# Optimization experiments

Measured on AMD Instinct MI355X. Metric: run time of the kernel, lower is better.

## Reference

```python
import jax, jax.numpy as jnp
import numpy as np

B, S, H = 4, 2048, 512
E, K = 8, 2
DFF = 4 * H


def setup_inputs() -> dict:
    key = jax.random.key(0)
    ks = jax.random.split(key, 6)
    x = jax.random.normal(ks[0], (B, S, H), dtype=jnp.float32)
    gate_W = jax.random.normal(ks[1], (H, E), dtype=jnp.float32) * 0.02
    gate_b = jnp.zeros((E,), dtype=jnp.float32)
    # Stacked expert params; Linear stored as [in, out] so y = x @ W + b
    W1 = jax.random.normal(ks[2], (E, H, DFF), dtype=jnp.float32) * 0.02
    b1 = jnp.zeros((E, DFF), dtype=jnp.float32)
    W2 = jax.random.normal(ks[3], (E, DFF, H), dtype=jnp.float32) * 0.02
    b2 = jnp.zeros((E, H), dtype=jnp.float32)
    return {"x": x, "gate_W": gate_W, "gate_b": gate_b,
            "W1": W1, "b1": b1, "W2": W2, "b2": b2}


def reference(x, gate_W, gate_b, W1, b1, W2, b2):
    bsz, seq, hid = x.shape
    flat = x.reshape(-1, hid)                       # [T, H]
    T = flat.shape[0]
    gate_logits = flat @ gate_W + gate_b            # [T, E]
    topk_vals, topk_idx = jax.lax.top_k(gate_logits, K)   # [T, K]
    topk_w = jax.nn.softmax(topk_vals, axis=-1)      # softmax over selected logits only

    # Scatter top-k weights into a dense per-token combine matrix [T, E];
    # zero weight where a token is not routed -> identical math to masked dispatch.
    combine = jnp.zeros((T, E), dtype=flat.dtype).at[
        jnp.arange(T)[:, None], topk_idx].add(topk_w)

    out_flat = jnp.zeros_like(flat)
    for e in range(E):  # fixed small loop over structurally distinct experts
        h = jax.nn.gelu(flat @ W1[e] + b1[e], approximate=False) @ W2[e] + b2[e]
        out_flat = out_flat + h * combine[:, e:e + 1]
    out = out_flat.reshape(bsz, seq, hid)

    probs = jax.nn.softmax(gate_logits, axis=-1).mean(axis=0)   # [E]
    l_aux = jnp.sum(probs * probs) * E
    expert_counts = jnp.zeros((E,), dtype=jnp.float32).at[
        topk_idx.reshape(-1)].add(1.0)
    return out, l_aux, expert_counts
```

## Files before the change

### kernel.cpp

```cpp
#include <hip/hip_runtime.h>
#include <math.h>

#define TOK 8192
#define HD  512
#define NE  8
#define DFF 2048

typedef __attribute__((ext_vector_type(8))) short bf16x8;
typedef __attribute__((ext_vector_type(4))) float floatx4;

__device__ inline unsigned short f2bf(float f) {
    union { float f; unsigned u; } v; v.f = f;
    unsigned r = v.u + 0x7FFFu + ((v.u >> 16) & 1u);
    return (unsigned short)(r >> 16);
}

__device__ inline float gelu_exact(float v) {
    return 0.5f * v * (1.f + erff(v * 0.70710678118654752f));
}

typedef __attribute__((address_space(1))) const unsigned int glb_u32;
typedef __attribute__((address_space(3))) unsigned int lds_u32;
__device__ __forceinline__ void gload16(const unsigned short* g, unsigned short* l) {
    __builtin_amdgcn_global_load_lds((glb_u32*)g, (lds_u32*)l, 16, 0, 0);
}

__global__ __launch_bounds__(256) void prep_kernel(
    const float* __restrict__ x, const float* __restrict__ gW, const float* __restrict__ gb,
    const float* __restrict__ W1, const float* __restrict__ W2,
    int* __restrict__ seg_count, float* __restrict__ probs_sum,
    int* __restrict__ seg_token, float* __restrict__ seg_w,
    unsigned short* __restrict__ xb,
    unsigned short* __restrict__ W1t, unsigned short* __restrict__ W2t)
{
    __shared__ __align__(16) char shraw[16896];
    int bid = blockIdx.x;
    int tid = threadIdx.x;

    if (bid >= 32) {
        int b = bid - 32;
        float (*tile)[65] = (float(*)[65])shraw;
        int z = b >> 8, rem = b & 255;
        int xq = rem & 31, yq = rem >> 5;
        const float* src; unsigned short* dst; int C, R, cb, rb;
        if (z < NE) {
            src = W1 + (size_t)z * HD * DFF; dst = W1t + (size_t)z * HD * DFF;
            R = HD; C = DFF; cb = xq; rb = yq;
        } else {
            int e = z - NE;
            src = W2 + (size_t)e * DFF * HD; dst = W2t + (size_t)e * DFF * HD;
            R = DFF; C = HD; cb = yq; rb = xq;
        }
        int c0 = cb * 64, r0 = rb * 64;
        int tq = (tid & 15) * 4, tr4 = tid >> 4;
        #pragma unroll
        for (int p = 0; p < 4; p++) {
            int rr = tr4 + 16 * p;
            float4 v = *(const float4*)&src[(size_t)(r0 + rr) * C + c0 + tq];
            tile[rr][tq + 0] = v.x; tile[rr][tq + 1] = v.y;
            tile[rr][tq + 2] = v.z; tile[rr][tq + 3] = v.w;
        }
        __syncthreads();
        int cc = tid >> 3, cq = (tid & 7) * 8;
        #pragma unroll
        for (int p = 0; p < 2; p++) {
            int c = cc + 32 * p;
            union { unsigned short s[8]; uint4 v; } u8;
            #pragma unroll
            for (int u = 0; u < 8; u++) u8.s[u] = f2bf(tile[cq + u][c]);
            *(uint4*)&dst[(size_t)(c0 + c) * R + r0 + cq] = u8.v;
        }
        return;
    }

    float* sW    = (float*)shraw;
    float* psum  = (float*)(shraw + 16384);
    int*   lcount = (int*)(shraw + 16448);
    int*   lbase  = (int*)(shraw + 16512);

    for (int i = tid; i < HD * NE; i += 256) sW[i] = gW[i];
    if (tid < NE) { psum[tid] = 0.f; lcount[tid] = 0; }
    __syncthreads();

    int t = bid * 256 + tid;
    float logit[NE];
    #pragma unroll
    for (int e = 0; e < NE; e++) logit[e] = gb[e];

    const float4* xr4 = reinterpret_cast<const float4*>(x + (size_t)t * HD);
    ushort4* xbw = reinterpret_cast<ushort4*>(xb + (size_t)t * HD);
    for (int j4 = 0; j4 < HD / 4; j4++) {
        float4 xv = xr4[j4];
        int j = j4 * 4;
        ushort4 o; o.x = f2bf(xv.x); o.y = f2bf(xv.y); o.z = f2bf(xv.z); o.w = f2bf(xv.w);
        xbw[j4] = o;
        #pragma unroll
        for (int e = 0; e < NE; e++) {
            logit[e] += xv.x * sW[(j + 0) * NE + e] + xv.y * sW[(j + 1) * NE + e]
                      + xv.z * sW[(j + 2) * NE + e] + xv.w * sW[(j + 3) * NE + e];
        }
    }

    float mx = logit[0];
    #pragma unroll
    for (int e = 1; e < NE; e++) mx = fmaxf(mx, logit[e]);
    float pe[NE]; float s = 0.f;
    #pragma unroll
    for (int e = 0; e < NE; e++) { pe[e] = expf(logit[e] - mx); s += pe[e]; }
    float inv = 1.f / s;
    int l = tid & 63;
    #pragma unroll
    for (int e = 0; e < NE; e++) {
        float v = pe[e] * inv;
        for (int off = 32; off; off >>= 1) v += __shfl_down(v, off);
        if (l == 0) atomicAdd(&psum[e], v);
    }

    int i0 = 0; float v0 = logit[0];
    #pragma unroll
    for (int e = 1; e < NE; e++) if (logit[e] > v0) { v0 = logit[e]; i0 = e; }
    int i1 = -1; float v1 = -3.4e38f;
    #pragma unroll
    for (int e = 0; e < NE; e++) if (e != i0 && logit[e] > v1) { v1 = logit[e]; i1 = e; }
    float e1 = expf(v1 - v0);
    float w0 = 1.f / (1.f + e1);
    float w1 = e1 / (1.f + e1);

    int r0 = atomicAdd(&lcount[i0], 1);
    int r1 = atomicAdd(&lcount[i1], 1);
    __syncthreads();
    if (tid < NE) lbase[tid] = atomicAdd(&seg_count[tid], lcount[tid]);
    __syncthreads();
    int p0 = lbase[i0] + r0;
    seg_token[i0 * TOK + p0] = t;
    seg_w[i0 * TOK + p0] = w0;
    int p1 = lbase[i1] + r1;
    seg_token[i1 * TOK + p1] = t | (1 << 16);
    seg_w[i1 * TOK + p1] = w1;

    __syncthreads();
    if (tid < NE) atomicAdd(&probs_sum[tid], psum[tid]);
}

#define TM  128
#define TN  128
#define BK  32

#define GEMM_BODY(NITV, SRC_A, SRC_B) \
    const int NIT = (NITV); \
    int rbuf = 0; \
    for (int k = 0; k < NIT; ++k) { \
        if (k + 1 < NIT) asm volatile("s_waitcnt vmcnt(8)" ::: "memory"); \
        else             asm volatile("s_waitcnt vmcnt(0)" ::: "memory"); \
        const unsigned short* A = &smem[w * 8192 + rbuf * 4096]; \
        const unsigned short* B = A + 2048; \
        bf16x8 a[4], b[4]; \
        _Pragma("unroll") \
        for (int i = 0; i < 4; i++) a[i] = *(const bf16x8*)&A[(16 * i + lr) * BK + rsw]; \
        _Pragma("unroll") \
        for (int j = 0; j < 4; j++) b[j] = *(const bf16x8*)&B[(16 * j + lr) * BK + rsw]; \
        asm volatile("s_waitcnt lgkmcnt(0)" ::: "memory"); \
        if (k + 2 < NIT) { \
            int ko = (k + 2) * BK; \
            unsigned short* da = &smem[w * 8192 + rbuf * 4096]; \
            _Pragma("unroll") \
            for (int s = 0; s < 4; s++) { \
                gload16(SRC_A + aofs[s] + ko, da + s * 512); \
                gload16(SRC_B + bofs[s] + ko, da + 2048 + s * 512); \
            } \
        } \
        __builtin_amdgcn_s_setprio(1); \
        _Pragma("unroll") \
        for (int i = 0; i < 4; i++) \
            _Pragma("unroll") \
            for (int j = 0; j < 4; j++) \
                acc[i][j] = __builtin_amdgcn_mfma_f32_16x16x32_bf16(a[i], b[j], acc[i][j], 0, 0, 0); \
        __builtin_amdgcn_s_setprio(0); \
        rbuf ^= 1; \
    }

__global__ __launch_bounds__(256) void gemm1_kernel(
    const unsigned short* __restrict__ xb,
    const unsigned short* __restrict__ W1t,
    const float* __restrict__ bias1,
    const int* __restrict__ seg_count, const float* __restrict__ probs_sum,
    const int* __restrict__ seg_token,
    unsigned short* __restrict__ hbuf,
    float* __restrict__ out_tail)
{
    int bid = blockIdx.x;
    int tid = threadIdx.x;

    if (bid == 0) {
        if (tid < NE) out_tail[1 + tid] = (float)seg_count[tid];
        else if (tid == 64) {
            float s = 0.f;
            #pragma unroll
            for (int e2 = 0; e2 < NE; e2++) {
                float p = probs_sum[e2] * (1.f / (float)TOK);
                s += p * p;
            }
            out_tail[0] = s * (float)NE;
        }
    }

    int e  = bid & 7;
    int r2 = bid >> 3;
    int nb = r2 & 15;
    int mb = r2 >> 4;
    int cnt = seg_count[e];
    if (mb * TM >= cnt) return;

    int off_e = 0;
    #pragma unroll
    for (int ee = 0; ee < NE; ee++) if (ee < e) off_e += (seg_count[ee] + 127) & ~127;
    int hb = off_e + mb * TM;

    __shared__ __align__(16) unsigned short smem[32768];

    int w = tid >> 6, l = tid & 63;
    int lr = l & 15, crow = (l >> 4) * 4;
    int wm = (w & 1) * 64, wn = (w >> 1) * 64;
    int rsw = ((l >> 4) ^ ((lr >> 1) & 3)) * 8;
    const unsigned short* w1e = W1t + (size_t)e * DFF * HD + (size_t)(nb * TN) * HD;

    unsigned csrc = (unsigned)(((l & 3) ^ ((l >> 3) & 3)) * 8);
    unsigned aofs[4], bofs[4];
    #pragma unroll
    for (int s = 0; s < 4; s++) {
        int rloc = s * 16 + (l >> 2);
        int gi = mb * TM + wm + rloc;
        int tok = seg_token[e * TOK + ((gi < cnt) ? gi : 0)] & 0xFFFF;
        aofs[s] = (unsigned)tok * HD + csrc;
        bofs[s] = (unsigned)((wn + rloc) * HD) + csrc;
    }

    floatx4 acc[4][4];
    #pragma unroll
    for (int i = 0; i < 4; i++)
        #pragma unroll
        for (int j = 0; j < 4; j++) acc[i][j] = (floatx4){0.f, 0.f, 0.f, 0.f};

    #pragma unroll
    for (int p = 0; p < 2; p++) {
        unsigned short* da = &smem[w * 8192 + p * 4096];
        #pragma unroll
        for (int s = 0; s < 4; s++) {
            gload16(xb  + aofs[s] + p * BK, da + s * 512);
            gload16(w1e + bofs[s] + p * BK, da + 2048 + s * 512);
        }
    }

    GEMM_BODY(HD / BK, xb, w1e)

    unsigned short* scr = &smem[w * 8192];
    #pragma unroll
    for (int j = 0; j < 4; j++) {
        float b1v = bias1[e * DFF + nb * TN + wn + 16 * j + lr];
        #pragma unroll
        for (int i = 0; i < 4; i++)
            #pragma unroll
            for (int rr = 0; rr < 4; rr++)
                scr[(16 * i + crow + rr) * 72 + 16 * j + lr] = f2bf(gelu_exact(acc[i][j][rr] + b1v));
    }
    int lh = l >> 3, ll = l & 7;
    #pragma unroll
    for (int k = 0; k < 8; k++) {
        uint4 v = *(const uint4*)&scr[(8 * k + lh) * 72 + ll * 8];
        int grow = hb + wm + 8 * k + lh;
        *(uint4*)&hbuf[(size_t)grow * DFF + nb * TN + wn + ll * 8] = v;
    }
}

__global__ __launch_bounds__(256) void gemm2_kernel(
    const unsigned short* __restrict__ hbuf,
    const unsigned short* __restrict__ W2t,
    const float* __restrict__ b2,
    const int* __restrict__ seg_count, const int* __restrict__ seg_token,
    const float* __restrict__ seg_w,
    float* __restrict__ pout,
    float* __restrict__ out,
    int use_pout)
{
    int bid = blockIdx.x;
    int tid = threadIdx.x;
    int e  = bid & 7;
    int r2 = bid >> 3;
    int nb = r2 & 3;
    int mb = r2 >> 2;
    int cnt = seg_count[e];
    if (mb * TM >= cnt) return;
    int off_e = 0;
    #pragma unroll
    for (int ee = 0; ee < NE; ee++) if (ee < e) off_e += (seg_count[ee] + 127) & ~127;
    int hb = off_e + mb * TM;

    __shared__ __align__(16) unsigned short smem[32768];

    int w = tid >> 6, l = tid & 63;
    int lr = l & 15, crow = (l >> 4) * 4;
    int wm = (w & 1) * 64, wn = (w >> 1) * 64;
    int rsw = ((l >> 4) ^ ((lr >> 1) & 3)) * 8;
    const unsigned short* w2e = W2t + (size_t)e * HD * DFF + (size_t)(nb * TN) * DFF;

    unsigned csrc = (unsigned)(((l & 3) ^ ((l >> 3) & 3)) * 8);
    unsigned aofs[4], bofs[4];
    #pragma unroll
    for (int s = 0; s < 4; s++) {
        int rloc = s * 16 + (l >> 2);
        aofs[s] = (unsigned)((hb + wm + rloc) * DFF) + csrc;
        bofs[s] = (unsigned)((wn + rloc) * DFF) + csrc;
    }

    floatx4 acc[4][4];
    #pragma unroll
    for (int i = 0; i < 4; i++)
        #pragma unroll
        for (int j = 0; j < 4; j++) acc[i][j] = (floatx4){0.f, 0.f, 0.f, 0.f};

    #pragma unroll
    for (int p = 0; p < 2; p++) {
        unsigned short* da = &smem[w * 8192 + p * 4096];
        #pragma unroll
        for (int s = 0; s < 4; s++) {
            gload16(hbuf + aofs[s] + p * BK, da + s * 512);
            gload16(w2e  + bofs[s] + p * BK, da + 2048 + s * 512);
        }
    }

    GEMM_BODY(DFF / BK, hbuf, w2e)

    int   raws[4][4];
    float wgts[4][4];
    #pragma unroll
    for (int i = 0; i < 4; i++)
        #pragma unroll
        for (int rr = 0; rr < 4; rr++) {
            int gi = mb * TM + wm + 16 * i + crow + rr;
            int idx = e * TOK + ((gi < cnt) ? gi : 0);
            raws[i][rr] = seg_token[idx];
            wgts[i][rr] = (gi < cnt) ? seg_w[idx] : 0.f;
        }

    if (use_pout) {
        #pragma unroll
        for (int j = 0; j < 4; j++) {
            int n = nb * TN + wn + 16 * j + lr;
            float b2v = b2[e * HD + n];
            #pragma unroll
            for (int i = 0; i < 4; i++)
                #pragma unroll
                for (int rr = 0; rr < 4; rr++) {
                    int gi = mb * TM + wm + 16 * i + crow + rr;
                    if (gi < cnt)
                        pout[((size_t)(raws[i][rr] & 0xFFFF) * 2 + (raws[i][rr] >> 16)) * HD + n] =
                            (acc[i][j][rr] + b2v) * wgts[i][rr];
                }
        }
    } else {
        #pragma unroll
        for (int j = 0; j < 4; j++) {
            int n = nb * TN + wn + 16 * j + lr;
            float b2v = b2[e * HD + n];
            #pragma unroll
            for (int i = 0; i < 4; i++)
                #pragma unroll
                for (int rr = 0; rr < 4; rr++)
                    atomicAdd(&out[(size_t)(raws[i][rr] & 0xFFFF) * HD + n],
                              (acc[i][j][rr] + b2v) * wgts[i][rr]);
        }
    }
}

__global__ __launch_bounds__(256) void combine_kernel(
    const float* __restrict__ pout, float* __restrict__ out)
{
    int idx = blockIdx.x * 256 + threadIdx.x;
    int t = idx >> 7;
    int c4 = idx & 127;
    const float4* p = (const float4*)pout;
    float4 a = p[((size_t)t * 2 + 0) * 128 + c4];
    float4 b = p[((size_t)t * 2 + 1) * 128 + c4];
    float4 r; r.x = a.x + b.x; r.y = a.y + b.y; r.z = a.z + b.z; r.w = a.w + b.w;
    ((float4*)out)[idx] = r;
}

#define BMT 64
#define FK  64
#define XS_LD 520
#define HS_LD 72

__global__ __launch_bounds__(256, 2) void ffn_fused_fallback(
    const unsigned short* __restrict__ xb,
    const unsigned short* __restrict__ W1t, const float* __restrict__ b1,
    const unsigned short* __restrict__ W2t, const float* __restrict__ b2,
    const int* __restrict__ seg_count, const int* __restrict__ seg_token,
    const float* __restrict__ seg_w, float* __restrict__ out)
{
    int bid = blockIdx.x;
    int e = bid & 7;
    int g = bid >> 3;
    int cnt = seg_count[e];
    int n0 = g * BMT;
    if (n0 >= cnt) return;
    int rows = min(BMT, cnt - n0);

    __shared__ unsigned short xs[BMT * XS_LD];
    __shared__ unsigned short hs[BMT * HS_LD];
    __shared__ int   tok_s[BMT];
    __shared__ float wgt_s[BMT];

    int tid = threadIdx.x;
    if (tid < BMT) {
        int idx = (tid < rows) ? (n0 + tid) : n0;
        tok_s[tid] = seg_token[e * TOK + idx] & 0xFFFF;
        wgt_s[tid] = (tid < rows) ? seg_w[e * TOK + idx] : 0.f;
    }
    __syncthreads();
    {
        int r = tid >> 2, q = tid & 3;
        const uint4* src = (const uint4*)(xb + (size_t)tok_s[r] * HD) + q * 16;
        uint4* dst = (uint4*)&xs[(size_t)r * XS_LD + q * 128];
        #pragma unroll
        for (int i = 0; i < 16; i++) dst[i] = src[i];
    }
    __syncthreads();

    int w = tid >> 6, l = tid & 63;
    int lr = l & 15, lk = (l >> 4) * 8, crow = (l >> 4) * 4;

    const unsigned short* w1e = W1t + (size_t)e * DFF * HD;
    const unsigned short* w2e = W2t + (size_t)e * HD * DFF;

    floatx4 acc2[4][8];
    #pragma unroll
    for (int i = 0; i < 4; i++)
        #pragma unroll
        for (int j = 0; j < 8; j++) acc2[i][j] = (floatx4){0.f, 0.f, 0.f, 0.f};

    for (int fc = 0; fc < DFF; fc += FK) {
        floatx4 acc1[4];
        #pragma unroll
        for (int t = 0; t < 4; t++) acc1[t] = (floatx4){0.f, 0.f, 0.f, 0.f};
        const unsigned short* w1c = w1e + (size_t)fc * HD;
        for (int ks = 0; ks < HD; ks += 32) {
            bf16x8 a = *(const bf16x8*)&xs[(16 * w + lr) * XS_LD + ks + lk];
            #pragma unroll
            for (int t = 0; t < 4; t++) {
                bf16x8 b = *(const bf16x8*)(w1c + (size_t)(16 * t + lr) * HD + ks + lk);
                acc1[t] = __builtin_amdgcn_mfma_f32_16x16x32_bf16(a, b, acc1[t], 0, 0, 0);
            }
        }
        __syncthreads();
        #pragma unroll
        for (int t = 0; t < 4; t++) {
            float b1v = b1[e * DFF + fc + 16 * t + lr];
            #pragma unroll
            for (int r = 0; r < 4; r++)
                hs[(16 * w + crow + r) * HS_LD + 16 * t + lr] = f2bf(gelu_exact(acc1[t][r] + b1v));
        }
        __syncthreads();
        #pragma unroll
        for (int ks = 0; ks < FK; ks += 32) {
            bf16x8 af[4];
            #pragma unroll
            for (int i = 0; i < 4; i++) af[i] = *(const bf16x8*)&hs[(16 * i + lr) * HS_LD + ks + lk];
            #pragma unroll
            for (int j = 0; j < 8; j++) {
                bf16x8 b = *(const bf16x8*)(w2e + (size_t)(128 * w + 16 * j + lr) * DFF + fc + ks + lk);
                #pragma unroll
                for (int i = 0; i < 4; i++)
                    acc2[i][j] = __builtin_amdgcn_mfma_f32_16x16x32_bf16(af[i], b, acc2[i][j], 0, 0, 0);
            }
        }
    }
    #pragma unroll
    for (int j = 0; j < 8; j++) {
        int n = 128 * w + 16 * j + lr;
        float b2v = b2[e * HD + n];
        #pragma unroll
        for (int i = 0; i < 4; i++)
            #pragma unroll
            for (int r = 0; r < 4; r++) {
                int m = 16 * i + crow + r;
                atomicAdd(&out[(size_t)tok_s[m] * HD + n], (acc2[i][j][r] + b2v) * wgt_s[m]);
            }
    }
}

__global__ void finalize_kernel(const int* __restrict__ seg_count,
                                const float* __restrict__ probs_sum,
                                float* __restrict__ out_tail)
{
    int tid = threadIdx.x;
    if (tid < NE) out_tail[1 + tid] = (float)seg_count[tid];
    if (tid == 0) {
        float s = 0.f;
        #pragma unroll
        for (int e = 0; e < NE; e++) {
            float p = probs_sum[e] * (1.f / (float)TOK);
            s += p * p;
        }
        out_tail[0] = s * (float)NE;
    }
}

extern "C" void kernel_launch(void* const* d_in, const int* in_sizes, int n_in,
                              void* d_out, int out_size, void* d_ws, size_t ws_size,
                              hipStream_t stream)
{
    const float* x  = (const float*)d_in[0];
    const float* gW = (const float*)d_in[1];
    const float* gb = (const float*)d_in[2];
    const float* W1 = (const float*)d_in[3];
    const float* b1 = (const float*)d_in[4];
    const float* W2 = (const float*)d_in[5];
    const float* b2 = (const float*)d_in[6];
    float* out = (float*)d_out;

    char* ws = (char*)d_ws;
    int*   seg_count = (int*)ws;
    float* probs_sum = (float*)(ws + 32);
    int*   seg_token = (int*)(ws + 4096);
    float* seg_w     = (float*)(ws + 4096 + (size_t)NE * TOK * 4);

    const size_t HBUF_BYTES = (size_t)17408 * DFF * 2;

    const size_t F_POUT = 0xA0000;
    const size_t F_XB   = (1u  << 20);
    const size_t F_W1T  = (9u  << 20);
    const size_t F_W2T  = F_POUT + (size_t)TOK * 2 * HD * 4;
    const size_t F_HBUF = F_W2T + ((size_t)NE * DFF * HD * 2);
    const size_t WS_FAST = F_HBUF + HBUF_BYTES;

    const size_t M_XB   = (1u  << 20);
    const size_t M_W1T  = (16u << 20);
    const size_t M_W2T  = (32u << 20);
    const size_t M_HBUF = (48u << 20);
    const size_t WS_MID = M_HBUF + HBUF_BYTES;

    hipMemsetAsync(d_ws, 0, 64, stream);

    if (ws_size >= WS_FAST) {
        unsigned short* xb   = (unsigned short*)(ws + F_XB);
        unsigned short* W1t  = (unsigned short*)(ws + F_W1T);
        unsigned short* W2t  = (unsigned short*)(ws + F_W2T);
        unsigned short* hbuf = (unsigned short*)(ws + F_HBUF);
        float*          pout = (float*)(ws + F_POUT);

        prep_kernel<<<4128, 256, 0, stream>>>(x, gW, gb, W1, W2,
                                              seg_count, probs_sum, seg_token, seg_w,
                                              xb, W1t, W2t);
        gemm1_kernel<<<NE * (DFF / TN) * 64, 256, 0, stream>>>(
            xb, W1t, b1, seg_count, probs_sum, seg_token, hbuf,
            out + (size_t)TOK * HD);
        gemm2_kernel<<<NE * (HD / TN) * 64, 256, 0, stream>>>(
            hbuf, W2t, b2, seg_count, seg_token, seg_w, pout, out, 1);
        combine_kernel<<<(TOK * HD / 4) / 256, 256, 0, stream>>>(pout, out);
    } else if (ws_size >= WS_MID) {
        unsigned short* xb   = (unsigned short*)(ws + M_XB);
        unsigned short* W1t  = (unsigned short*)(ws + M_W1T);
        unsigned short* W2t  = (unsigned short*)(ws + M_W2T);
        unsigned short* hbuf = (unsigned short*)(ws + M_HBUF);

        hipMemsetAsync(d_out, 0, (size_t)TOK * HD * sizeof(float), stream);
        prep_kernel<<<4128, 256, 0, stream>>>(x, gW, gb, W1, W2,
                                              seg_count, probs_sum, seg_token, seg_w,
                                              xb, W1t, W2t);
        gemm1_kernel<<<NE * (DFF / TN) * 64, 256, 0, stream>>>(
            xb, W1t, b1, seg_count, probs_sum, seg_token, hbuf,
            out + (size_t)TOK * HD);
        gemm2_kernel<<<NE * (HD / TN) * 64, 256, 0, stream>>>(
            hbuf, W2t, b2, seg_count, seg_token, seg_w, (float*)ws, out, 0);
    } else {
        unsigned short* xb   = (unsigned short*)(ws + M_XB);
        unsigned short* W1t  = (unsigned short*)(ws + M_W1T);
        unsigned short* W2t  = (unsigned short*)(ws + M_W2T);

        hipMemsetAsync(d_out, 0, (size_t)TOK * HD * sizeof(float), stream);
        prep_kernel<<<4128, 256, 0, stream>>>(x, gW, gb, W1, W2,
                                              seg_count, probs_sum, seg_token, seg_w,
                                              xb, W1t, W2t);
        finalize_kernel<<<1, 64, 0, stream>>>(seg_count, probs_sum, out + (size_t)TOK * HD);
        ffn_fused_fallback<<<(TOK / BMT) * NE, 256, 0, stream>>>(
            xb, W1t, b1, W2t, b2, seg_count, seg_token, seg_w, out);
    }
}
```

Measured before the change: 342.3 us.

## Move W2 transpose-convert from prep kernel into extra gemm1 blocks

```diff
diff --git a/kernel.cpp b/kernel.cpp
--- a/kernel.cpp
+++ b/kernel.cpp
@@ -145,6 +145,7 @@
 #define TM  128
 #define TN  128
 #define BK  32
+#define G1_GRID (NE * (DFF / TN) * 64)
 
 #define GEMM_BODY(NITV, SRC_A, SRC_B) \
     const int NIT = (NITV); \
@@ -186,10 +187,44 @@
     const int* __restrict__ seg_count, const float* __restrict__ probs_sum,
     const int* __restrict__ seg_token,
     unsigned short* __restrict__ hbuf,
-    float* __restrict__ out_tail)
+    float* __restrict__ out_tail,
+    const float* __restrict__ W2src,
+    unsigned short* __restrict__ W2t)
 {
     int bid = blockIdx.x;
     int tid = threadIdx.x;
+
+    __shared__ __align__(16) unsigned short smem[32768];
+
+    if (bid >= G1_GRID) {
+        int b = bid - G1_GRID;
+        float (*tile)[65] = (float(*)[65])smem;
+        int e = b >> 8, rem = b & 255;
+        int xq = rem & 31, yq = rem >> 5;
+        const float* src = W2src + (size_t)e * DFF * HD;
+        unsigned short* dst = W2t + (size_t)e * DFF * HD;
+        const int R = DFF, C = HD;
+        int c0 = yq * 64, r0 = xq * 64;
+        int tq = (tid & 15) * 4, tr4 = tid >> 4;
+        #pragma unroll
+        for (int p = 0; p < 4; p++) {
+            int rr = tr4 + 16 * p;
+            float4 v = *(const float4*)&src[(size_t)(r0 + rr) * C + c0 + tq];
+            tile[rr][tq + 0] = v.x; tile[rr][tq + 1] = v.y;
+            tile[rr][tq + 2] = v.z; tile[rr][tq + 3] = v.w;
+        }
+        __syncthreads();
+        int cc = tid >> 3, cq = (tid & 7) * 8;
+        #pragma unroll
+        for (int p = 0; p < 2; p++) {
+            int c = cc + 32 * p;
+            union { unsigned short s[8]; uint4 v; } u8;
+            #pragma unroll
+            for (int u = 0; u < 8; u++) u8.s[u] = f2bf(tile[cq + u][c]);
+            *(uint4*)&dst[(size_t)(c0 + c) * R + r0 + cq] = u8.v;
+        }
+        return;
+    }
 
     if (bid == 0) {
         if (tid < NE) out_tail[1 + tid] = (float)seg_count[tid];
@@ -215,8 +250,6 @@
     #pragma unroll
     for (int ee = 0; ee < NE; ee++) if (ee < e) off_e += (seg_count[ee] + 127) & ~127;
     int hb = off_e + mb * TM;
-
-    __shared__ __align__(16) unsigned short smem[32768];
 
     int w = tid >> 6, l = tid & 63;
     int lr = l & 15, crow = (l >> 4) * 4;
@@ -548,12 +581,12 @@
         unsigned short* hbuf = (unsigned short*)(ws + F_HBUF);
         float*          pout = (float*)(ws + F_POUT);
 
-        prep_kernel<<<4128, 256, 0, stream>>>(x, gW, gb, W1, W2,
+        prep_kernel<<<2080, 256, 0, stream>>>(x, gW, gb, W1, W2,
                                               seg_count, probs_sum, seg_token, seg_w,
                                               xb, W1t, W2t);
-        gemm1_kernel<<<NE * (DFF / TN) * 64, 256, 0, stream>>>(
+        gemm1_kernel<<<G1_GRID + 2048, 256, 0, stream>>>(
             xb, W1t, b1, seg_count, probs_sum, seg_token, hbuf,
-            out + (size_t)TOK * HD);
+            out + (size_t)TOK * HD, W2, W2t);
         gemm2_kernel<<<NE * (HD / TN) * 64, 256, 0, stream>>>(
             hbuf, W2t, b2, seg_count, seg_token, seg_w, pout, out, 1);
         combine_kernel<<<(TOK * HD / 4) / 256, 256, 0, stream>>>(pout, out);
@@ -564,12 +597,12 @@
         unsigned short* hbuf = (unsigned short*)(ws + M_HBUF);
 
         hipMemsetAsync(d_out, 0, (size_t)TOK * HD * sizeof(float), stream);
-        prep_kernel<<<4128, 256, 0, stream>>>(x, gW, gb, W1, W2,
+        prep_kernel<<<2080, 256, 0, stream>>>(x, gW, gb, W1, W2,
                                               seg_count, probs_sum, seg_token, seg_w,
                                               xb, W1t, W2t);
-        gemm1_kernel<<<NE * (DFF / TN) * 64, 256, 0, stream>>>(
+        gemm1_kernel<<<G1_GRID + 2048, 256, 0, stream>>>(
             xb, W1t, b1, seg_count, probs_sum, seg_token, hbuf,
-            out + (size_t)TOK * HD);
+            out + (size_t)TOK * HD, W2, W2t);
         gemm2_kernel<<<NE * (HD / TN) * 64, 256, 0, stream>>>(
             hbuf, W2t, b2, seg_count, seg_token, seg_w, (float*)ws, out, 0);
     } else {
```

Result: no change. 339.7 us (-0.8%).

## Shrink expert GEMM tiles to 64x64 single-wave blocks

Applied to the files above, without the earlier changes.

```diff
diff --git a/kernel.cpp b/kernel.cpp
--- a/kernel.cpp
+++ b/kernel.cpp
@@ -142,9 +142,9 @@
     if (tid < NE) atomicAdd(&probs_sum[tid], psum[tid]);
 }
 
-#define TM  128
-#define TN  128
 #define BK  32
+#define G1_GRID (NE * (DFF / 64) * 128)
+#define G2_GRID (NE * (HD  / 64) * 128)
 
 #define GEMM_BODY(NITV, SRC_A, SRC_B) \
     const int NIT = (NITV); \
@@ -152,7 +152,7 @@
     for (int k = 0; k < NIT; ++k) { \
         if (k + 1 < NIT) asm volatile("s_waitcnt vmcnt(8)" ::: "memory"); \
         else             asm volatile("s_waitcnt vmcnt(0)" ::: "memory"); \
-        const unsigned short* A = &smem[w * 8192 + rbuf * 4096]; \
+        const unsigned short* A = &smem[rbuf * 4096]; \
         const unsigned short* B = A + 2048; \
         bf16x8 a[4], b[4]; \
         _Pragma("unroll") \
@@ -162,7 +162,7 @@
         asm volatile("s_waitcnt lgkmcnt(0)" ::: "memory"); \
         if (k + 2 < NIT) { \
             int ko = (k + 2) * BK; \
-            unsigned short* da = &smem[w * 8192 + rbuf * 4096]; \
+            unsigned short* da = &smem[rbuf * 4096]; \
             _Pragma("unroll") \
             for (int s = 0; s < 4; s++) { \
                 gload16(SRC_A + aofs[s] + ko, da + s * 512); \
@@ -179,7 +179,7 @@
         rbuf ^= 1; \
     }
 
-__global__ __launch_bounds__(256) void gemm1_kernel(
+__global__ __launch_bounds__(64) void gemm1_kernel(
     const unsigned short* __restrict__ xb,
     const unsigned short* __restrict__ W1t,
     const float* __restrict__ bias1,
@@ -193,7 +193,7 @@
 
     if (bid == 0) {
         if (tid < NE) out_tail[1 + tid] = (float)seg_count[tid];
-        else if (tid == 64) {
+        else if (tid == 32) {
             float s = 0.f;
             #pragma unroll
             for (int e2 = 0; e2 < NE; e2++) {
@@ -206,33 +206,32 @@
 
     int e  = bid & 7;
     int r2 = bid >> 3;
-    int nb = r2 & 15;
-    int mb = r2 >> 4;
+    int nb = r2 & 31;
+    int mb = r2 >> 5;
     int cnt = seg_count[e];
-    if (mb * TM >= cnt) return;
+    if (mb * 64 >= cnt) return;
 
     int off_e = 0;
     #pragma unroll
     for (int ee = 0; ee < NE; ee++) if (ee < e) off_e += (seg_count[ee] + 127) & ~127;
-    int hb = off_e + mb * TM;
-
-    __shared__ __align__(16) unsigned short smem[32768];
-
-    int w = tid >> 6, l = tid & 63;
+    int hb = off_e + mb * 64;
+
+    __shared__ __align__(16) unsigned short smem[8192];
+
+    int l = tid;
     int lr = l & 15, crow = (l >> 4) * 4;
-    int wm = (w & 1) * 64, wn = (w >> 1) * 64;
     int rsw = ((l >> 4) ^ ((lr >> 1) & 3)) * 8;
-    const unsigned short* w1e = W1t + (size_t)e * DFF * HD + (size_t)(nb * TN) * HD;
+    const unsigned short* w1e = W1t + (size_t)e * DFF * HD + (size_t)(nb * 64) * HD;
 
     unsigned csrc = (unsigned)(((l & 3) ^ ((l >> 3) & 3)) * 8);
     unsigned aofs[4], bofs[4];
     #pragma unroll
     for (int s = 0; s < 4; s++) {
         int rloc = s * 16 + (l >> 2);
-        int gi = mb * TM + wm + rloc;
+        int gi = mb * 64 + rloc;
         int tok = seg_token[e * TOK + ((gi < cnt) ? gi : 0)] & 0xFFFF;
         aofs[s] = (unsigned)tok * HD + csrc;
-        bofs[s] = (unsigned)((wn + rloc) * HD) + csrc;
+        bofs[s] = (unsigned)(rloc * HD) + csrc;
     }
 
     floatx4 acc[4][4];
@@ -243,7 +242,7 @@
 
     #pragma unroll
     for (int p = 0; p < 2; p++) {
-        unsigned short* da = &smem[w * 8192 + p * 4096];
+        unsigned short* da = &smem[p * 4096];
         #pragma unroll
         for (int s = 0; s < 4; s++) {
             gload16(xb  + aofs[s] + p * BK, da + s * 512);
@@ -253,10 +252,10 @@
 
     GEMM_BODY(HD / BK, xb, w1e)
 
-    unsigned short* scr = &smem[w * 8192];
+    unsigned short* scr = smem;
     #pragma unroll
     for (int j = 0; j < 4; j++) {
-        float b1v = bias1[e * DFF + nb * TN + wn + 16 * j + lr];
+        float b1v = bias1[e * DFF + nb * 64 + 16 * j + lr];
         #pragma unroll
         for (int i = 0; i < 4; i++)
             #pragma unroll
@@ -267,12 +266,12 @@
     #pragma unroll
     for (int k = 0; k < 8; k++) {
         uint4 v = *(const uint4*)&scr[(8 * k + lh) * 72 + ll * 8];
-        int grow = hb + wm + 8 * k + lh;
-        *(uint4*)&hbuf[(size_t)grow * DFF + nb * TN + wn + ll * 8] = v;
-    }
-}
-
-__global__ __launch_bounds__(256) void gemm2_kernel(
+        int grow = hb + 8 * k + lh;
+        *(uint4*)&hbuf[(size_t)grow * DFF + nb * 64 + ll * 8] = v;
+    }
+}
+
+__global__ __launch_bounds__(64) void gemm2_kernel(
     const unsigned short* __restrict__ hbuf,
     const unsigned short* __restrict__ W2t,
     const float* __restrict__ b2,
@@ -286,30 +285,29 @@
     int tid = threadIdx.x;
     int e  = bid & 7;
     int r2 = bid >> 3;
-    int nb = r2 & 3;
-    int mb = r2 >> 2;
+    int nb = r2 & 7;
+    int mb = r2 >> 3;
     int cnt = seg_count[e];
-    if (mb * TM >= cnt) return;
+    if (mb * 64 >= cnt) return;
     int off_e = 0;
     #pragma unroll
     for (int ee = 0; ee < NE; ee++) if (ee < e) off_e += (seg_count[ee] + 127) & ~127;
-    int hb = off_e + mb * TM;
-
-    __shared__ __align__(16) unsigned short smem[32768];
-
-    int w = tid >> 6, l = tid & 63;
+    int hb = off_e + mb * 64;
+
+    __shared__ __align__(16) unsigned short smem[8192];
+
+    int l = tid;
     int lr = l & 15, crow = (l >> 4) * 4;
-    int wm = (w & 1) * 64, wn = (w >> 1) * 64;
     int rsw = ((l >> 4) ^ ((lr >> 1) & 3)) * 8;
-    const unsigned short* w2e = W2t + (size_t)e * HD * DFF + (size_t)(nb * TN) * DFF;
+    const unsigned short* w2e = W2t + (size_t)e * HD * DFF + (size_t)(nb * 64) * DFF;
 
     unsigned csrc = (unsigned)(((l & 3) ^ ((l >> 3) & 3)) * 8);
     unsigned aofs[4], bofs[4];
     #pragma unroll
     for (int s = 0; s < 4; s++) {
         int rloc = s * 16 + (l >> 2);
-        aofs[s] = (unsigned)((hb + wm + rloc) * DFF) + csrc;
-        bofs[s] = (unsigned)((wn + rloc) * DFF) + csrc;
+        aofs[s] = (unsigned)((hb + rloc) * DFF) + csrc;
+        bofs[s] = (unsigned)(rloc * DFF) + csrc;
     }
 
     floatx4 acc[4][4];
@@ -320,7 +318,7 @@
 
     #pragma unroll
     for (int p = 0; p < 2; p++) {
-        unsigned short* da = &smem[w * 8192 + p * 4096];
+        unsigned short* da = &smem[p * 4096];
         #pragma unroll
         for (int s = 0; s < 4; s++) {
             gload16(hbuf + aofs[s] + p * BK, da + s * 512);
@@ -336,7 +334,7 @@
     for (int i = 0; i < 4; i++)
         #pragma unroll
         for (int rr = 0; rr < 4; rr++) {
-            int gi = mb * TM + wm + 16 * i + crow + rr;
+            int gi = mb * 64 + 16 * i + crow + rr;
             int idx = e * TOK + ((gi < cnt) ? gi : 0);
             raws[i][rr] = seg_token[idx];
             wgts[i][rr] = (gi < cnt) ? seg_w[idx] : 0.f;
@@ -345,13 +343,13 @@
     if (use_pout) {
         #pragma unroll
         for (int j = 0; j < 4; j++) {
-            int n = nb * TN + wn + 16 * j + lr;
+            int n = nb * 64 + 16 * j + lr;
             float b2v = b2[e * HD + n];
             #pragma unroll
             for (int i = 0; i < 4; i++)
                 #pragma unroll
                 for (int rr = 0; rr < 4; rr++) {
-                    int gi = mb * TM + wm + 16 * i + crow + rr;
+                    int gi = mb * 64 + 16 * i + crow + rr;
                     if (gi < cnt)
                         pout[((size_t)(raws[i][rr] & 0xFFFF) * 2 + (raws[i][rr] >> 16)) * HD + n] =
                             (acc[i][j][rr] + b2v) * wgts[i][rr];
@@ -360,7 +358,7 @@
     } else {
         #pragma unroll
         for (int j = 0; j < 4; j++) {
-            int n = nb * TN + wn + 16 * j + lr;
+            int n = nb * 64 + 16 * j + lr;
             float b2v = b2[e * HD + n];
             #pragma unroll
             for (int i = 0; i < 4; i++)
@@ -551,10 +549,10 @@
         prep_kernel<<<4128, 256, 0, stream>>>(x, gW, gb, W1, W2,
                                               seg_count, probs_sum, seg_token, seg_w,
                                               xb, W1t, W2t);
-        gemm1_kernel<<<NE * (DFF / TN) * 64, 256, 0, stream>>>(
+        gemm1_kernel<<<G1_GRID, 64, 0, stream>>>(
             xb, W1t, b1, seg_count, probs_sum, seg_token, hbuf,
             out + (size_t)TOK * HD);
-        gemm2_kernel<<<NE * (HD / TN) * 64, 256, 0, stream>>>(
+        gemm2_kernel<<<G2_GRID, 64, 0, stream>>>(
             hbuf, W2t, b2, seg_count, seg_token, seg_w, pout, out, 1);
         combine_kernel<<<(TOK * HD / 4) / 256, 256, 0, stream>>>(pout, out);
     } else if (ws_size >= WS_MID) {
@@ -567,10 +565,10 @@
         prep_kernel<<<4128, 256, 0, stream>>>(x, gW, gb, W1, W2,
                                               seg_count, probs_sum, seg_token, seg_w,
                                               xb, W1t, W2t);
-        gemm1_kernel<<<NE * (DFF / TN) * 64, 256, 0, stream>>>(
+        gemm1_kernel<<<G1_GRID, 64, 0, stream>>>(
             xb, W1t, b1, seg_count, probs_sum, seg_token, hbuf,
             out + (size_t)TOK * HD);
-        gemm2_kernel<<<NE * (HD / TN) * 64, 256, 0, stream>>>(
+        gemm2_kernel<<<G2_GRID, 64, 0, stream>>>(
             hbuf, W2t, b2, seg_count, seg_token, seg_w, (float*)ws, out, 0);
     } else {
         unsigned short* xb   = (unsigned short*)(ws + M_XB);
```

New measurement: 342.8 us. About the same (+0.1%).
